# Performance work log

Measured on AMD Instinct MI355X. Metric: run time of the kernel, lower is better.

The kernel has to match this reference:

```python
import jax, jax.numpy as jnp
import numpy as np
from jax import lax

B, N, C = 8, 16384, 4
NUM_GROUPS = 128
GROUP_SIZE = 32
GROUP_RADIUS = 0.1
UPSCALE_K = 128
OVERLAP_FACTOR = 0.7


def setup_inputs() -> dict:
    key = jax.random.key(0)
    k1, k2 = jax.random.split(key)
    # xyz in [0,1]^3, energy in [0,1] at channel 3
    points = jax.random.uniform(k1, (B, N, C), dtype=jnp.float32)
    lengths = jax.random.randint(k2, (B,), N // 2, N + 1).astype(jnp.int32)
    return {"points": points, "lengths": lengths}


def _fps(xyz, lengths, K):
    """Farthest point sampling. xyz: (B,N,3) -> centers (B,K,3), idx (B,K)."""
    B_, N_, _ = xyz.shape
    valid = jnp.arange(N_)[None, :] < lengths[:, None]          # (B,N)
    mind0 = jnp.where(valid, jnp.inf, -jnp.inf)                 # running min dist
    start = jnp.zeros((B_,), jnp.int32)                         # fixed start point
    batch = jnp.arange(B_)

    def step(carry, _):
        mind, cur = carry
        c = xyz[batch, cur]                                     # (B,3)
        d = jnp.sum((xyz - c[:, None, :]) ** 2, axis=-1)        # (B,N)
        mind = jnp.minimum(mind, jnp.where(valid, d, -jnp.inf))
        nxt = jnp.argmax(mind, axis=1).astype(jnp.int32)
        return (mind, nxt), cur

    _, idxs = lax.scan(step, (mind0, start), None, length=K)
    idxs = idxs.T                                               # (B,K)
    centers = xyz[batch[:, None], idxs]                         # (B,K,3)
    return centers, idxs


def _cnms(centers, radius, overlap_factor):
    """Greedy cluster-NMS over FPS-ordered centers. Returns keep mask (B,G)."""
    B_, G, _ = centers.shape
    d2 = jnp.sum((centers[:, :, None, :] - centers[:, None, :, :]) ** 2, axis=-1)
    thr = (2.0 * radius * (1.0 - overlap_factor)) ** 2          # spheres overlap > factor

    def step(keep, j):
        conflict = jnp.any(keep & (d2[:, j, :] < thr), axis=-1)
        keep = keep.at[:, j].set(~conflict)
        return keep, None

    keep, _ = lax.scan(step, jnp.zeros((B_, G), bool), jnp.arange(G))
    return keep


def _ball_query(centers, xyz, lengths, retain, K, radius):
    """First-K points within radius of each center (pytorch3d semantics); -1 pad."""
    N_ = xyz.shape[1]
    d2 = jnp.sum((centers[:, :, None, :] - xyz[:, None, :, :]) ** 2, axis=-1)  # (B,G,N)
    in_len = (jnp.arange(N_)[None, :] < lengths[:, None])[:, None, :]
    valid = (d2 <= radius * radius) & in_len & retain[:, :, None]
    # pick the K smallest point indices among valid ones -> "first K found"
    key_ = jnp.where(valid, jnp.arange(N_, dtype=jnp.int32)[None, None, :], N_)
    negv, _ = lax.top_k(-key_, K)                               # (B,G,K)
    idx = -negv
    return jnp.where(idx == N_, -1, idx)


def reference(points, lengths):
    xyz = points[..., :3]
    centers, _ = _fps(xyz, lengths, NUM_GROUPS)                 # (B,G,3)
    retain = _cnms(centers, GROUP_RADIUS, OVERLAP_FACTOR)       # (B,G)
    idx = _ball_query(centers, xyz, lengths, retain, UPSCALE_K, GROUP_RADIUS)

    # select_topk_by_energy (energies_idx = 3)
    batch = jnp.arange(points.shape[0])[:, None, None]
    invalid = idx == -1
    energies = jnp.where(invalid, -jnp.inf, points[batch, jnp.clip(idx, 0), 3])
    topv, topi = lax.top_k(energies, GROUP_SIZE)                # (B,G,K_new)
    tidx = jnp.take_along_axis(idx, topi, axis=2)
    tidx = jnp.where(jnp.isneginf(topv), -1, tidx)

    # fill_empty_indices: replace -1 with the group's first index
    fidx = jnp.where(tidx == -1, tidx[:, :, :1], tidx)

    # masked_gather: -1 -> gather 0 then zero out
    groups = points[batch, jnp.clip(fidx, 0)]                   # (B,G,K,C)
    groups = jnp.where((fidx == -1)[..., None], 0.0, groups)

    group_lengths = jnp.sum(jnp.all(tidx != -1, axis=2), axis=1)  # (B,)
    embedding_mask = jnp.arange(NUM_GROUPS)[None, :] < group_lengths[:, None]

    # center xyz channels, then scale ALL channels by radius (as in source)
    groups = groups.at[..., :3].add(-centers[:, :, None, :])
    groups = groups / GROUP_RADIUS
    return groups, centers, embedding_mask
```

## Files before the change

### kernel.cpp

```cpp
#include <hip/hip_runtime.h>
#include <math.h>

#define B_ 8
#define N_ 16384
#define G_ 128
#define GS_ 32
#define UK_ 128
#define FPS_T 1024
#define FPS_W 16
#define FPS_BLK 4
#define SLICE (N_ / FPS_BLK)
#define PPT (SLICE / FPS_T)
#define BQ_T 512
#define BQ_W 8

__device__ __forceinline__ float dist2(float x, float y, float z,
                                       float cx, float cy, float cz) {
    float dx = __fsub_rn(x, cx);
    float dy = __fsub_rn(y, cy);
    float dz = __fsub_rn(z, cz);
    return __fadd_rn(__fadd_rn(__fmul_rn(dx, dx), __fmul_rn(dy, dy)),
                     __fmul_rn(dz, dz));
}

__device__ __forceinline__ unsigned long long shfl_xor_u64(unsigned long long v, int m) {
    int lo = __shfl_xor((int)(unsigned)(v & 0xffffffffull), m);
    int hi = __shfl_xor((int)(unsigned)(v >> 32), m);
    return ((unsigned long long)(unsigned)hi << 32) | (unsigned)lo;
}

__device__ __forceinline__ unsigned long long umax64(unsigned long long a,
                                                     unsigned long long b) {
    return a > b ? a : b;
}

__device__ __forceinline__ unsigned wave_umax_bcast(unsigned v) {
    unsigned t;
    t = (unsigned)__builtin_amdgcn_update_dpp(0, (int)v, 0x111, 0xf, 0xf, false); v = v > t ? v : t;
    t = (unsigned)__builtin_amdgcn_update_dpp(0, (int)v, 0x112, 0xf, 0xf, false); v = v > t ? v : t;
    t = (unsigned)__builtin_amdgcn_update_dpp(0, (int)v, 0x114, 0xf, 0xf, false); v = v > t ? v : t;
    t = (unsigned)__builtin_amdgcn_update_dpp(0, (int)v, 0x118, 0xf, 0xf, false); v = v > t ? v : t;
    t = (unsigned)__builtin_amdgcn_update_dpp(0, (int)v, 0x142, 0xa, 0xf, false); v = v > t ? v : t;
    t = (unsigned)__builtin_amdgcn_update_dpp(0, (int)v, 0x143, 0xc, 0xf, false); v = v > t ? v : t;
    return (unsigned)__builtin_amdgcn_readlane((int)v, 63);
}
__device__ __forceinline__ unsigned wave_umin_bcast(unsigned v) {
    unsigned t;
    t = (unsigned)__builtin_amdgcn_update_dpp(-1, (int)v, 0x111, 0xf, 0xf, false); v = v < t ? v : t;
    t = (unsigned)__builtin_amdgcn_update_dpp(-1, (int)v, 0x112, 0xf, 0xf, false); v = v < t ? v : t;
    t = (unsigned)__builtin_amdgcn_update_dpp(-1, (int)v, 0x114, 0xf, 0xf, false); v = v < t ? v : t;
    t = (unsigned)__builtin_amdgcn_update_dpp(-1, (int)v, 0x118, 0xf, 0xf, false); v = v < t ? v : t;
    t = (unsigned)__builtin_amdgcn_update_dpp(-1, (int)v, 0x142, 0xa, 0xf, false); v = v < t ? v : t;
    t = (unsigned)__builtin_amdgcn_update_dpp(-1, (int)v, 0x143, 0xc, 0xf, false); v = v < t ? v : t;
    return (unsigned)__builtin_amdgcn_readlane((int)v, 63);
}

__global__ void init_kernel(unsigned long long* __restrict__ slots,
                            int* __restrict__ gl) {
    int t = threadIdx.x;
#pragma unroll
    for (int i = 0; i < (B_ * G_ * FPS_BLK) / 1024; i++)
        slots[i * 1024 + t] = 0ull;
    if (t < B_) gl[t] = 0;
}

__global__ __launch_bounds__(FPS_T, 4) void fps_cnms_kernel(
    const float4* __restrict__ pts, const int* __restrict__ lengths,
    float* __restrict__ centers_out, int* __restrict__ keep_out,
    unsigned long long* __restrict__ slots) {
    const int b = blockIdx.x & 7;
    const int slice = blockIdx.x >> 3;
    const int t = threadIdx.x;
    const int lane = t & 63;
    const int wv = t >> 6;
    const int len = lengths[b];
    const float4* p = pts + (size_t)b * N_;
    const int base = slice * SLICE;

    __shared__ float4 s_xy4[SLICE / 2];
    __shared__ __align__(16) unsigned long long s_part[FPS_W];
    __shared__ int s_bcn[2];
    __shared__ float s_cen[G_][3];

    float zs[PPT], mind[PPT];
#pragma unroll
    for (int i2 = 0; i2 < PPT / 2; i2++) {
        int nA = base + (2 * i2) * FPS_T + t;
        int nB = base + (2 * i2 + 1) * FPS_T + t;
        float4 qA = p[nA];
        float4 qB = p[nB];
        s_xy4[i2 * FPS_T + t] = make_float4(qA.x, qA.y, qB.x, qB.y);
        zs[2 * i2]     = qA.z;
        zs[2 * i2 + 1] = qB.z;
        mind[2 * i2]     = (nA < len) ? INFINITY : -INFINITY;
        mind[2 * i2 + 1] = (nB < len) ? INFINITY : -INFINITY;
    }
    __syncthreads();

    int n = 0;
    for (int k = 0; k < G_; k++) {
        float4 c = p[n];
        float cx = c.x, cy = c.y, cz = c.z;
        if (slice == 0 && t == 0) {
            centers_out[(b * G_ + k) * 3 + 0] = cx;
            centers_out[(b * G_ + k) * 3 + 1] = cy;
            centers_out[(b * G_ + k) * 3 + 2] = cz;
            s_cen[k][0] = cx; s_cen[k][1] = cy; s_cen[k][2] = cz;
        }
        if (k == G_ - 1) break;

        float bv = -INFINITY;
        int bn = 0x7fffffff;
#pragma unroll
        for (int i2 = 0; i2 < PPT / 2; i2++) {
            float4 xy = s_xy4[i2 * FPS_T + t];
            float dA = dist2(xy.x, xy.y, zs[2 * i2],     cx, cy, cz);
            float dB = dist2(xy.z, xy.w, zs[2 * i2 + 1], cx, cy, cz);
            float mA = fminf(mind[2 * i2], dA);
            float mB = fminf(mind[2 * i2 + 1], dB);
            mind[2 * i2] = mA;
            mind[2 * i2 + 1] = mB;
            if (mA > bv) { bv = mA; bn = base + (2 * i2) * FPS_T + t; }
            if (mB > bv) { bv = mB; bn = base + (2 * i2 + 1) * FPS_T + t; }
        }
        unsigned u = __float_as_uint(bv);
        u = (u & 0x80000000u) ? ~u : (u | 0x80000000u);

        unsigned wmax = wave_umax_bcast(u);
        unsigned ik = (u == wmax) ? (unsigned)bn : 0xffffffffu;
        unsigned wbn = wave_umin_bcast(ik);

        if (lane == 0)
            s_part[wv] = ((unsigned long long)wmax << 32) | (unsigned)(~wbn);
        __syncthreads();

        if (wv == 0) {
            unsigned long long kk = s_part[lane & 15];
#pragma unroll
            for (int off = 8; off; off >>= 1)
                kk = umax64(kk, shfl_xor_u64(kk, off));

            unsigned long long* slot = slots + ((size_t)b * G_ + k) * FPS_BLK;
            if (lane == 0)
                __hip_atomic_store(&slot[slice], kk, __ATOMIC_RELAXED,
                                   __HIP_MEMORY_SCOPE_AGENT);
            unsigned long long v = kk;
            if (lane < FPS_BLK && lane != slice) {
                do {
                    v = __hip_atomic_load(&slot[lane], __ATOMIC_RELAXED,
                                          __HIP_MEMORY_SCOPE_AGENT);
                } while (v == 0ull);
            }
            unsigned long long m = umax64(v, shfl_xor_u64(v, 1));
            m = umax64(m, shfl_xor_u64(m, 2));
            if (lane == 0)
                s_bcn[k & 1] = (int)(~(unsigned)(m & 0xffffffffull));
        }
        __syncthreads();
        n = s_bcn[k & 1];
    }

    if (slice == 0 && t < 64) {
        const float THR = (float)((2.0 * 0.1 * (1.0 - 0.7)) * (2.0 * 0.1 * (1.0 - 0.7)));
        float ax = s_cen[t][0],      ay = s_cen[t][1],      az = s_cen[t][2];
        float ex = s_cen[t + 64][0], ey = s_cen[t + 64][1], ez = s_cen[t + 64][2];
        bool k0 = false, k1 = false;
        for (int j = 0; j < G_; j++) {
            float jx = s_cen[j][0], jy = s_cen[j][1], jz = s_cen[j][2];
            bool c0 = k0 && (dist2(ax, ay, az, jx, jy, jz) < THR);
            bool c1 = k1 && (dist2(ex, ey, ez, jx, jy, jz) < THR);
            bool conflict = __any(c0 || c1);
            if (j == t)      k0 = !conflict;
            if (j == t + 64) k1 = !conflict;
        }
        keep_out[b * G_ + t]      = k0 ? 1 : 0;
        keep_out[b * G_ + t + 64] = k1 ? 1 : 0;
    }
}

__global__ __launch_bounds__(BQ_T) void group_kernel(
    const float4* __restrict__ pts, const int* __restrict__ lengths,
    const float* __restrict__ centers, const int* __restrict__ keep,
    float* __restrict__ groups_out, int* __restrict__ gl) {
    const int bid = blockIdx.x;
    const int b = bid >> 7;
    const int t = threadIdx.x;
    const int lane = t & 63;
    const int wv = t >> 6;

    const float cx = centers[bid * 3 + 0];
    const float cy = centers[bid * 3 + 1];
    const float cz = centers[bid * 3 + 2];
    float4* out4 = (float4*)(groups_out + (size_t)bid * GS_ * 4);

    if (!keep[bid]) {
        if (t < GS_) {
            float4 o;
            o.x = __fdiv_rn(__fsub_rn(0.f, cx), 0.1f);
            o.y = __fdiv_rn(__fsub_rn(0.f, cy), 0.1f);
            o.z = __fdiv_rn(__fsub_rn(0.f, cz), 0.1f);
            o.w = 0.f;
            out4[t] = o;
        }
        return;
    }

    __shared__ int   s_widx[BQ_W][UK_];
    __shared__ float s_wen[BQ_W][UK_];
    __shared__ int   s_wcnt[BQ_W];
    __shared__ int   s_list[UK_];
    __shared__ float s_en[UK_];
    __shared__ int   s_ord[GS_];

    const int len = lengths[b];
    const float R2 = (float)(0.1 * 0.1);
    const float4* p = pts + (size_t)b * N_;

    {
        const int base0 = wv * (N_ / BQ_W);
        int cnt = 0;
        for (int it = 0; it < (N_ / BQ_W) / 64; it++) {
            int n = base0 + it * 64 + lane;
            float4 q = p[n];
            float d2 = dist2(q.x, q.y, q.z, cx, cy, cz);
            bool pred = (n < len) && (d2 <= R2);
            unsigned long long m = __ballot(pred);
            int prefix = __popcll(m & ((1ull << lane) - 1ull));
            int slot = cnt + prefix;
            if (pred && slot < UK_) { s_widx[wv][slot] = n; s_wen[wv][slot] = q.w; }
            cnt += __popcll(m);
        }
        if (lane == 0) s_wcnt[wv] = (cnt < UK_) ? cnt : UK_;
    }
    __syncthreads();

    int M = 0;
#pragma unroll
    for (int w = 0; w < BQ_W; w++) M += s_wcnt[w];
    if (M > UK_) M = UK_;

    if (t < UK_ && t < M) {
        int j = t, w = 0;
        while (w < BQ_W - 1 && j >= s_wcnt[w]) { j -= s_wcnt[w]; w++; }
        s_list[t] = s_widx[w][j];
        s_en[t]   = s_wen[w][j];
    }
    __syncthreads();

    if (wv == 0) {
        float v0 = (lane < M) ? s_en[lane] : -INFINITY;
        float v1 = (lane + 64 < M) ? s_en[lane + 64] : -INFINITY;
        for (int k = 0; k < GS_; k++) {
            float bv; int bs;
            if (v0 >= v1) { bv = v0; bs = lane; }
            else          { bv = v1; bs = lane + 64; }
#pragma unroll
            for (int off = 32; off; off >>= 1) {
                float ov = __shfl_xor(bv, off);
                int   os = __shfl_xor(bs, off);
                bool tk = (ov > bv) || (ov == bv && os < bs);
                bv = tk ? ov : bv; bs = tk ? os : bs;
            }
            if (lane == 0) s_ord[k] = (bv == -INFINITY) ? -1 : bs;
            if (bs == lane)           v0 = -INFINITY;
            else if (bs == lane + 64) v1 = -INFINITY;
        }
    }
    __syncthreads();

    if (t < GS_) {
        int o0 = s_ord[0];
        int first = (o0 >= 0) ? s_list[o0] : -1;
        int ok = s_ord[t];
        int ti = (ok >= 0) ? s_list[ok] : -1;
        int f = (ti == -1) ? first : ti;
        float px = 0.f, py = 0.f, pz = 0.f, pw = 0.f;
        if (f >= 0) { float4 q = p[f]; px = q.x; py = q.y; pz = q.z; pw = q.w; }
        float4 o;
        o.x = __fdiv_rn(__fsub_rn(px, cx), 0.1f);
        o.y = __fdiv_rn(__fsub_rn(py, cy), 0.1f);
        o.z = __fdiv_rn(__fsub_rn(pz, cz), 0.1f);
        o.w = __fdiv_rn(pw, 0.1f);
        out4[t] = o;
    }
    if (t == 0 && M >= GS_) atomicAdd(&gl[b], 1);
}

__global__ void mask_kernel(const int* __restrict__ gl, float* __restrict__ mask_out) {
    int t = threadIdx.x;
    int b = t >> 7, g = t & 127;
    mask_out[t] = (g < gl[b]) ? 1.0f : 0.0f;
}

extern "C" void kernel_launch(void* const* d_in, const int* in_sizes, int n_in,
                              void* d_out, int out_size, void* d_ws, size_t ws_size,
                              hipStream_t stream) {
    const float4* pts = (const float4*)d_in[0];
    const int* lengths = (const int*)d_in[1];
    float* out = (float*)d_out;
    float* groups = out;
    float* centers = out + (size_t)B_ * G_ * GS_ * 4;
    float* mask = centers + (size_t)B_ * G_ * 3;
    unsigned long long* slots = (unsigned long long*)d_ws;
    int* keep = (int*)(slots + B_ * G_ * FPS_BLK);
    int* gl = keep + B_ * G_;

    hipLaunchKernelGGL(init_kernel, dim3(1), dim3(1024), 0, stream, slots, gl);
    hipLaunchKernelGGL(fps_cnms_kernel, dim3(B_ * FPS_BLK), dim3(FPS_T), 0, stream,
                       pts, lengths, centers, keep, slots);
    hipLaunchKernelGGL(group_kernel, dim3(B_ * G_), dim3(BQ_T), 0, stream,
                       pts, lengths, centers, keep, groups, gl);
    hipLaunchKernelGGL(mask_kernel, dim3(1), dim3(B_ * G_), 0, stream, gl, mask);
}
```

Before: 299.3 us.

## Run FPS in one block per batch with packed-FP32 math and 64-bit DPP argmax

Replaces the four-block-per-batch FPS, which coordinated through global-memory atomic slots and spin-waits, with a single 1024-thread block per batch that keeps all 16 points per thread in registers. Distance math uses v_pk_add/v_pk_mul packed FP32, and the argmax packs value and index into a 64-bit key reduced by DPP, leaving one barrier per iteration via double-buffered shared partials. This removes the cross-block global sync latency and the slot-initialisation pass, at the cost of 4x fewer CUs on the FPS stage and more register pressure. Packed add of negated centers may change rounding relative to the reference subtraction only if the ISA behaves differently, which it should not.

```diff
diff --git a/kernel.cpp b/kernel.cpp
--- a/kernel.cpp
+++ b/kernel.cpp
@@ -8,11 +8,24 @@
 #define UK_ 128
 #define FPS_T 1024
 #define FPS_W 16
-#define FPS_BLK 4
-#define SLICE (N_ / FPS_BLK)
-#define PPT (SLICE / FPS_T)
+#define PPT 16
 #define BQ_T 512
 #define BQ_W 8
+
+typedef float v2f __attribute__((ext_vector_type(2)));
+
+#define PK_ADD(d, a, b) asm("v_pk_add_f32 %0, %1, %2" : "=v"(d) : "v"(a), "v"(b))
+#define PK_MUL(d, a, b) asm("v_pk_mul_f32 %0, %1, %2" : "=v"(d) : "v"(a), "v"(b))
+
+#define DPP64_MAXSTEP(vv, ctrl, rmask)                                          \
+  {                                                                             \
+    unsigned _lo = (unsigned)__builtin_amdgcn_update_dpp(                       \
+        0, (int)(unsigned)((vv) & 0xffffffffull), (ctrl), (rmask), 0xf, false); \
+    unsigned _hi = (unsigned)__builtin_amdgcn_update_dpp(                       \
+        0, (int)(unsigned)((vv) >> 32), (ctrl), (rmask), 0xf, false);           \
+    unsigned long long _tv = ((unsigned long long)_hi << 32) | _lo;             \
+    if (_tv > (vv)) (vv) = _tv;                                                 \
+  }
 
 __device__ __forceinline__ float dist2(float x, float y, float z,
                                        float cx, float cy, float cz) {
@@ -23,144 +36,106 @@
                      __fmul_rn(dz, dz));
 }
 
-__device__ __forceinline__ unsigned long long shfl_xor_u64(unsigned long long v, int m) {
-    int lo = __shfl_xor((int)(unsigned)(v & 0xffffffffull), m);
-    int hi = __shfl_xor((int)(unsigned)(v >> 32), m);
-    return ((unsigned long long)(unsigned)hi << 32) | (unsigned)lo;
-}
-
-__device__ __forceinline__ unsigned long long umax64(unsigned long long a,
-                                                     unsigned long long b) {
-    return a > b ? a : b;
-}
-
-__device__ __forceinline__ unsigned wave_umax_bcast(unsigned v) {
-    unsigned t;
-    t = (unsigned)__builtin_amdgcn_update_dpp(0, (int)v, 0x111, 0xf, 0xf, false); v = v > t ? v : t;
-    t = (unsigned)__builtin_amdgcn_update_dpp(0, (int)v, 0x112, 0xf, 0xf, false); v = v > t ? v : t;
-    t = (unsigned)__builtin_amdgcn_update_dpp(0, (int)v, 0x114, 0xf, 0xf, false); v = v > t ? v : t;
-    t = (unsigned)__builtin_amdgcn_update_dpp(0, (int)v, 0x118, 0xf, 0xf, false); v = v > t ? v : t;
-    t = (unsigned)__builtin_amdgcn_update_dpp(0, (int)v, 0x142, 0xa, 0xf, false); v = v > t ? v : t;
-    t = (unsigned)__builtin_amdgcn_update_dpp(0, (int)v, 0x143, 0xc, 0xf, false); v = v > t ? v : t;
-    return (unsigned)__builtin_amdgcn_readlane((int)v, 63);
-}
-__device__ __forceinline__ unsigned wave_umin_bcast(unsigned v) {
-    unsigned t;
-    t = (unsigned)__builtin_amdgcn_update_dpp(-1, (int)v, 0x111, 0xf, 0xf, false); v = v < t ? v : t;
-    t = (unsigned)__builtin_amdgcn_update_dpp(-1, (int)v, 0x112, 0xf, 0xf, false); v = v < t ? v : t;
-    t = (unsigned)__builtin_amdgcn_update_dpp(-1, (int)v, 0x114, 0xf, 0xf, false); v = v < t ? v : t;
-    t = (unsigned)__builtin_amdgcn_update_dpp(-1, (int)v, 0x118, 0xf, 0xf, false); v = v < t ? v : t;
-    t = (unsigned)__builtin_amdgcn_update_dpp(-1, (int)v, 0x142, 0xa, 0xf, false); v = v < t ? v : t;
-    t = (unsigned)__builtin_amdgcn_update_dpp(-1, (int)v, 0x143, 0xc, 0xf, false); v = v < t ? v : t;
-    return (unsigned)__builtin_amdgcn_readlane((int)v, 63);
-}
-
-__global__ void init_kernel(unsigned long long* __restrict__ slots,
-                            int* __restrict__ gl) {
+__global__ void init_kernel(int* __restrict__ gl) {
     int t = threadIdx.x;
-#pragma unroll
-    for (int i = 0; i < (B_ * G_ * FPS_BLK) / 1024; i++)
-        slots[i * 1024 + t] = 0ull;
     if (t < B_) gl[t] = 0;
 }
 
 __global__ __launch_bounds__(FPS_T, 4) void fps_cnms_kernel(
     const float4* __restrict__ pts, const int* __restrict__ lengths,
-    float* __restrict__ centers_out, int* __restrict__ keep_out,
-    unsigned long long* __restrict__ slots) {
-    const int b = blockIdx.x & 7;
-    const int slice = blockIdx.x >> 3;
+    float* __restrict__ centers_out, int* __restrict__ keep_out) {
+    const int b = blockIdx.x;
     const int t = threadIdx.x;
     const int lane = t & 63;
     const int wv = t >> 6;
     const int len = lengths[b];
     const float4* p = pts + (size_t)b * N_;
-    const int base = slice * SLICE;
-
-    __shared__ float4 s_xy4[SLICE / 2];
-    __shared__ __align__(16) unsigned long long s_part[FPS_W];
-    __shared__ int s_bcn[2];
+
+    __shared__ __align__(16) unsigned long long s_part[2][FPS_W];
     __shared__ float s_cen[G_][3];
 
-    float zs[PPT], mind[PPT];
-#pragma unroll
-    for (int i2 = 0; i2 < PPT / 2; i2++) {
-        int nA = base + (2 * i2) * FPS_T + t;
-        int nB = base + (2 * i2 + 1) * FPS_T + t;
+    v2f xp[PPT / 2], yp[PPT / 2], zp[PPT / 2];
+    float mind[PPT];
+#pragma unroll
+    for (int j = 0; j < PPT / 2; j++) {
+        int nA = (2 * j) * FPS_T + t;
+        int nB = nA + FPS_T;
         float4 qA = p[nA];
         float4 qB = p[nB];
-        s_xy4[i2 * FPS_T + t] = make_float4(qA.x, qA.y, qB.x, qB.y);
-        zs[2 * i2]     = qA.z;
-        zs[2 * i2 + 1] = qB.z;
-        mind[2 * i2]     = (nA < len) ? INFINITY : -INFINITY;
-        mind[2 * i2 + 1] = (nB < len) ? INFINITY : -INFINITY;
-    }
-    __syncthreads();
+        v2f xx, yy, zz;
+        xx.x = qA.x; xx.y = qB.x;
+        yy.x = qA.y; yy.y = qB.y;
+        zz.x = qA.z; zz.y = qB.z;
+        xp[j] = xx; yp[j] = yy; zp[j] = zz;
+        mind[2 * j]     = (nA < len) ? INFINITY : -INFINITY;
+        mind[2 * j + 1] = (nB < len) ? INFINITY : -INFINITY;
+    }
 
     int n = 0;
     for (int k = 0; k < G_; k++) {
         float4 c = p[n];
-        float cx = c.x, cy = c.y, cz = c.z;
-        if (slice == 0 && t == 0) {
-            centers_out[(b * G_ + k) * 3 + 0] = cx;
-            centers_out[(b * G_ + k) * 3 + 1] = cy;
-            centers_out[(b * G_ + k) * 3 + 2] = cz;
-            s_cen[k][0] = cx; s_cen[k][1] = cy; s_cen[k][2] = cz;
+        if (t == 0) {
+            centers_out[(b * G_ + k) * 3 + 0] = c.x;
+            centers_out[(b * G_ + k) * 3 + 1] = c.y;
+            centers_out[(b * G_ + k) * 3 + 2] = c.z;
+            s_cen[k][0] = c.x; s_cen[k][1] = c.y; s_cen[k][2] = c.z;
         }
         if (k == G_ - 1) break;
 
+        float ncx = -c.x, ncy = -c.y, ncz = -c.z;
+        v2f cX, cY, cZ;
+        cX.x = ncx; cX.y = ncx;
+        cY.x = ncy; cY.y = ncy;
+        cZ.x = ncz; cZ.y = ncz;
+
         float bv = -INFINITY;
-        int bn = 0x7fffffff;
-#pragma unroll
-        for (int i2 = 0; i2 < PPT / 2; i2++) {
-            float4 xy = s_xy4[i2 * FPS_T + t];
-            float dA = dist2(xy.x, xy.y, zs[2 * i2],     cx, cy, cz);
-            float dB = dist2(xy.z, xy.w, zs[2 * i2 + 1], cx, cy, cz);
-            float mA = fminf(mind[2 * i2], dA);
-            float mB = fminf(mind[2 * i2 + 1], dB);
-            mind[2 * i2] = mA;
-            mind[2 * i2 + 1] = mB;
-            if (mA > bv) { bv = mA; bn = base + (2 * i2) * FPS_T + t; }
-            if (mB > bv) { bv = mB; bn = base + (2 * i2 + 1) * FPS_T + t; }
-        }
+        int bi = 0;
+#pragma unroll
+        for (int j = 0; j < PPT / 2; j++) {
+            v2f dx, dy, dz, qx, qy, qz, s0, d2v;
+            PK_ADD(dx, xp[j], cX);
+            PK_ADD(dy, yp[j], cY);
+            PK_ADD(dz, zp[j], cZ);
+            PK_MUL(qx, dx, dx);
+            PK_MUL(qy, dy, dy);
+            PK_MUL(qz, dz, dz);
+            PK_ADD(s0, qx, qy);
+            PK_ADD(d2v, s0, qz);
+            float mA = fminf(mind[2 * j],     d2v.x);
+            float mB = fminf(mind[2 * j + 1], d2v.y);
+            mind[2 * j] = mA;
+            mind[2 * j + 1] = mB;
+            if (mA > bv) { bv = mA; bi = 2 * j; }
+            if (mB > bv) { bv = mB; bi = 2 * j + 1; }
+        }
+
         unsigned u = __float_as_uint(bv);
         u = (u & 0x80000000u) ? ~u : (u | 0x80000000u);
-
-        unsigned wmax = wave_umax_bcast(u);
-        unsigned ik = (u == wmax) ? (unsigned)bn : 0xffffffffu;
-        unsigned wbn = wave_umin_bcast(ik);
-
-        if (lane == 0)
-            s_part[wv] = ((unsigned long long)wmax << 32) | (unsigned)(~wbn);
+        int bn = (bi << 10) | t;
+        unsigned long long v = ((unsigned long long)u << 32) | (unsigned)(~bn);
+
+        DPP64_MAXSTEP(v, 0x111, 0xf);
+        DPP64_MAXSTEP(v, 0x112, 0xf);
+        DPP64_MAXSTEP(v, 0x114, 0xf);
+        DPP64_MAXSTEP(v, 0x118, 0xf);
+        DPP64_MAXSTEP(v, 0x142, 0xa);
+        DPP64_MAXSTEP(v, 0x143, 0xc);
+        if (lane == 63) s_part[k & 1][wv] = v;
         __syncthreads();
 
-        if (wv == 0) {
-            unsigned long long kk = s_part[lane & 15];
-#pragma unroll
-            for (int off = 8; off; off >>= 1)
-                kk = umax64(kk, shfl_xor_u64(kk, off));
-
-            unsigned long long* slot = slots + ((size_t)b * G_ + k) * FPS_BLK;
-            if (lane == 0)
-                __hip_atomic_store(&slot[slice], kk, __ATOMIC_RELAXED,
-                                   __HIP_MEMORY_SCOPE_AGENT);
-            unsigned long long v = kk;
-            if (lane < FPS_BLK && lane != slice) {
-                do {
-                    v = __hip_atomic_load(&slot[lane], __ATOMIC_RELAXED,
-                                          __HIP_MEMORY_SCOPE_AGENT);
-                } while (v == 0ull);
-            }
-            unsigned long long m = umax64(v, shfl_xor_u64(v, 1));
-            m = umax64(m, shfl_xor_u64(m, 2));
-            if (lane == 0)
-                s_bcn[k & 1] = (int)(~(unsigned)(m & 0xffffffffull));
-        }
-        __syncthreads();
-        n = s_bcn[k & 1];
-    }
-
-    if (slice == 0 && t < 64) {
+        unsigned long long m = s_part[k & 1][lane & 15];
+        DPP64_MAXSTEP(m, 0x111, 0xf);
+        DPP64_MAXSTEP(m, 0x112, 0xf);
+        DPP64_MAXSTEP(m, 0x114, 0xf);
+        DPP64_MAXSTEP(m, 0x118, 0xf);
+        unsigned wlo = (unsigned)__builtin_amdgcn_readlane(
+            (int)(unsigned)(m & 0xffffffffull), 15);
+        n = (int)(~wlo);
+    }
+
+    __syncthreads();
+
+    if (t < 64) {
         const float THR = (float)((2.0 * 0.1 * (1.0 - 0.7)) * (2.0 * 0.1 * (1.0 - 0.7)));
         float ax = s_cen[t][0],      ay = s_cen[t][1],      az = s_cen[t][2];
         float ex = s_cen[t + 64][0], ey = s_cen[t + 64][1], ez = s_cen[t + 64][2];
@@ -301,13 +276,12 @@
     float* groups = out;
     float* centers = out + (size_t)B_ * G_ * GS_ * 4;
     float* mask = centers + (size_t)B_ * G_ * 3;
-    unsigned long long* slots = (unsigned long long*)d_ws;
-    int* keep = (int*)(slots + B_ * G_ * FPS_BLK);
+    int* keep = (int*)d_ws;
     int* gl = keep + B_ * G_;
 
-    hipLaunchKernelGGL(init_kernel, dim3(1), dim3(1024), 0, stream, slots, gl);
-    hipLaunchKernelGGL(fps_cnms_kernel, dim3(B_ * FPS_BLK), dim3(FPS_T), 0, stream,
-                       pts, lengths, centers, keep, slots);
+    hipLaunchKernelGGL(init_kernel, dim3(1), dim3(64), 0, stream, gl);
+    hipLaunchKernelGGL(fps_cnms_kernel, dim3(B_), dim3(FPS_T), 0, stream,
+                       pts, lengths, centers, keep);
     hipLaunchKernelGGL(group_kernel, dim3(B_ * G_), dim3(BQ_T), 0, stream,
                        pts, lengths, centers, keep, groups, gl);
     hipLaunchKernelGGL(mask_kernel, dim3(1), dim3(B_ * G_), 0, stream, gl, mask);
```

Measured after the change: 346.3 us. 1.16x slower.
